# Kernel optimization log

Measured on AMD Instinct MI355X. Metric: run time of the kernel, lower is better.

Reference implementation:

```python
import jax, jax.numpy as jnp
import numpy as np
import math

D_MODEL = 1024
NUM_NEURONS = 2048
LUT_SIZE = 4096
TWO_PI = 2.0 * math.pi


def lut_sin_cos(theta, sin_table, cos_table):
    # Interpolated periodic table lookup over [0, 2*pi)
    n = sin_table.shape[0]
    pos = (theta / TWO_PI) * n
    pos = jnp.mod(pos, n)
    i0 = jnp.floor(pos).astype(jnp.int32)
    frac = pos - i0.astype(theta.dtype)
    i1 = jnp.mod(i0 + 1, n)
    s = sin_table[i0] * (1.0 - frac) + sin_table[i1] * frac
    c = cos_table[i0] * (1.0 - frac) + cos_table[i1] * frac
    return s, c


def setup_inputs() -> dict:
    key = jax.random.key(0)
    ks = jax.random.split(key, 10)
    B = 64
    x_real = jax.random.normal(ks[0], (B, D_MODEL), jnp.float32)
    x_imag = jax.random.normal(ks[1], (B, D_MODEL), jnp.float32)
    t = jax.random.uniform(ks[2], (B,), jnp.float32)
    # xavier_uniform with gain=0.5 for linear weights
    def xavier(k, shape, gain):
        fan_out, fan_in = shape
        a = gain * math.sqrt(6.0 / (fan_in + fan_out))
        return jax.random.uniform(k, shape, jnp.float32, -a, a)
    ic_w = xavier(ks[3], (D_MODEL, 2 * D_MODEL), 0.5)
    ic_b = jnp.zeros((D_MODEL,), jnp.float32)
    W = jax.random.normal(ks[4], (NUM_NEURONS, D_MODEL), jnp.float32) * 0.02
    Bp = jnp.zeros((NUM_NEURONS, D_MODEL), jnp.float32)
    attn_cos = jnp.ones((NUM_NEURONS, D_MODEL), jnp.float32)
    attn_sin = jnp.ones((NUM_NEURONS, D_MODEL), jnp.float32)
    wr = xavier(ks[5], (D_MODEL, NUM_NEURONS), 0.5)
    wi = xavier(ks[6], (D_MODEL, NUM_NEURONS), 0.5)
    grid = jnp.arange(LUT_SIZE, dtype=jnp.float32) * (TWO_PI / LUT_SIZE)
    sin_table = jnp.sin(grid)
    cos_table = jnp.cos(grid)
    return {"x_real": x_real, "x_imag": x_imag, "t": t,
            "ic_w": ic_w, "ic_b": ic_b, "W": W, "Bp": Bp,
            "attn_cos": attn_cos, "attn_sin": attn_sin,
            "wr": wr, "wi": wi,
            "sin_table": sin_table, "cos_table": cos_table}


def reference(x_real, x_imag, t, ic_w, ic_b, W, Bp, attn_cos, attn_sin, wr, wi, sin_table, cos_table):
    x_combined = jnp.concatenate([x_real, x_imag], axis=-1)          # [B, 2D]
    x_collapsed = x_combined @ ic_w.T + ic_b                          # [B, D]
    wavelength = 1.0 + jnp.abs(W)                                     # [N, D]
    theta = x_collapsed[:, None, :] / wavelength + Bp + t[:, None, None]  # [B, N, D]
    sin_t, cos_t = lut_sin_cos(theta, sin_table, cos_table)
    cos_sum = jnp.einsum('bnd,nd->bn', cos_t, attn_cos)               # fused weight+reduce
    sin_sum = jnp.einsum('bnd,nd->bn', sin_t, attn_sin)
    out_real = jax.nn.silu(cos_sum @ wr.T)                            # [B, D]
    out_imag = jax.nn.silu(sin_sum @ wi.T)
    return out_real, out_imag
```

## Files before the change

kernel.cpp:

```cpp
#include <hip/hip_runtime.h>
#include <stdint.h>

#define DM 1024
#define NN 2048
#define BB 64

static constexpr float INV2PI = 0.15915494309189535f;

__device__ __forceinline__ uint32_t bf16r(float x) {
  uint32_t b = __float_as_uint(x);
  b += 0x7fffu + ((b >> 16) & 1u);
  return b >> 16;
}

__global__ __launch_bounds__(256) void k0_prep(
    const float* __restrict__ xr, const float* __restrict__ xi,
    float* __restrict__ xcombP)
{
  __shared__ float tile[64][65];
  int bid = blockIdx.x;
  int t = threadIdx.x;
  int k0 = bid * 64;
  const float* src = (k0 < 1024) ? xr : xi;
  int koff = k0 & 1023;
  int c = t & 63, rl = t >> 6;
#pragma unroll
  for (int i = 0; i < 16; ++i) {
    int b = rl * 16 + i;
    tile[b][c] = src[b * 1024 + koff + c];
  }
  __syncthreads();
  float2* out2 = (float2*)xcombP;
  int bl = t & 63, kp = t >> 6;
#pragma unroll
  for (int i = 0; i < 8; ++i) {
    int kl = (kp * 8 + i) * 2;
    float2 v = make_float2(tile[bl][kl], tile[bl][kl + 1]);
    out2[(size_t)((k0 + kl) >> 1) * 64 + bl] = v;
  }
}

__global__ __launch_bounds__(1024) void k1_collapse(
    const float* __restrict__ xcombP, const float* __restrict__ icw,
    const float* __restrict__ icb, const float* __restrict__ W,
    uint32_t* __restrict__ xcp, float* __restrict__ rinv)
{
  __shared__ float part[16][4][64];
  int bid = blockIdx.x;
  int t = threadIdx.x;
  if (bid >= 256) {
    int j = bid - 256;
    const float4* W4 = (const float4*)W;
    float4* R4 = (float4*)rinv;
    int base = j * 2048 + t;
#pragma unroll
    for (int i = 0; i < 2; ++i) {
      int idx = base + i * 1024;
      float4 w = W4[idx];
      float4 r;
      r.x = 1.0f / (1.0f + fabsf(w.x));
      r.y = 1.0f / (1.0f + fabsf(w.y));
      r.z = 1.0f / (1.0f + fabsf(w.z));
      r.w = 1.0f / (1.0f + fabsf(w.w));
      R4[idx] = r;
    }
    return;
  }
  int d0 = bid * 4;
  int wave = __builtin_amdgcn_readfirstlane((int)(t >> 6));
  int lane = t & 63;
  const float2* P2 = (const float2*)xcombP;
  float acc[4] = {0.f, 0.f, 0.f, 0.f};
  int kbase = wave * 128;
  for (int kk = 0; kk < 128; kk += 4) {
    int k = kbase + kk;
    float2 xa = P2[(size_t)(k >> 1) * 64 + lane];
    float2 xb = P2[(size_t)((k >> 1) + 1) * 64 + lane];
#pragma unroll
    for (int r = 0; r < 4; ++r) {
      float4 w = *(const float4*)(icw + (size_t)(d0 + r) * 2048 + k);
      acc[r] = fmaf(w.x, xa.x, acc[r]);
      acc[r] = fmaf(w.y, xa.y, acc[r]);
      acc[r] = fmaf(w.z, xb.x, acc[r]);
      acc[r] = fmaf(w.w, xb.y, acc[r]);
    }
  }
#pragma unroll
  for (int r = 0; r < 4; ++r) part[wave][r][lane] = acc[r];
  __syncthreads();
  if (t < 128) {
    int pj = t >> 6;
    int b = t & 63;
    float s0 = 0.f, s1 = 0.f;
#pragma unroll
    for (int w = 0; w < 16; ++w) {
      s0 += part[w][2 * pj][b];
      s1 += part[w][2 * pj + 1][b];
    }
    float x0 = (s0 + icb[d0 + 2 * pj]) * INV2PI;
    float x1 = (s1 + icb[d0 + 2 * pj + 1]) * INV2PI;
    uint32_t u = bf16r(x0) | (bf16r(x1) << 16);
    xcp[(size_t)((d0 >> 1) + pj) * 64 + b] = u;
  }
}

#define K2_STEP(r4, b4, a4, s4, xu0, xu1)                                 \
  do {                                                                     \
    float x0 = __uint_as_float((xu0) << 16);                               \
    float x1 = __uint_as_float((xu0) & 0xffff0000u);                       \
    float x2 = __uint_as_float((xu1) << 16);                               \
    float x3 = __uint_as_float((xu1) & 0xffff0000u);                       \
    float rv0 = fmaf(x0, (r4).x, fmaf((b4).x, INV2PI, t2));                \
    accc0 = fmaf(__builtin_amdgcn_cosf(rv0), (a4).x, accc0);               \
    accs0 = fmaf(__builtin_amdgcn_sinf(rv0), (s4).x, accs0);               \
    float rv1 = fmaf(x1, (r4).y, fmaf((b4).y, INV2PI, t2));                \
    accc1 = fmaf(__builtin_amdgcn_cosf(rv1), (a4).y, accc1);               \
    accs1 = fmaf(__builtin_amdgcn_sinf(rv1), (s4).y, accs1);               \
    float rv2 = fmaf(x2, (r4).z, fmaf((b4).z, INV2PI, t2));                \
    accc0 = fmaf(__builtin_amdgcn_cosf(rv2), (a4).z, accc0);               \
    accs0 = fmaf(__builtin_amdgcn_sinf(rv2), (s4).z, accs0);               \
    float rv3 = fmaf(x3, (r4).w, fmaf((b4).w, INV2PI, t2));                \
    accc1 = fmaf(__builtin_amdgcn_cosf(rv3), (a4).w, accc1);               \
    accs1 = fmaf(__builtin_amdgcn_sinf(rv3), (s4).w, accs1);               \
  } while (0)

__global__ __launch_bounds__(512) void k2_resonant(
    const uint32_t* __restrict__ xcp, const float* __restrict__ rinv,
    const float* __restrict__ Bp, const float* __restrict__ ac,
    const float* __restrict__ as_, const float* __restrict__ tin,
    uint32_t* __restrict__ cssP)
{
  __shared__ __align__(16) uint32_t xlds[64][64];
  __shared__ __align__(16) float plds[2][2][8][4][64];
  int wave = __builtin_amdgcn_readfirstlane((int)(threadIdx.x >> 6));
  int lane = threadIdx.x & 63;
  int bid = blockIdx.x;
  int q = bid & 7;
  int n0 = (bid >> 3) * 16 + wave;
  float t2 = tin[lane] * INV2PI;

  const char* xsrc = (const char*)(xcp + (size_t)q * 64 * 64);
  char* xdst = (char*)&xlds[0][0];
#pragma unroll
  for (int r = 0; r < 2; ++r) {
    int j = wave * 2 + r;
    __builtin_amdgcn_global_load_lds(
        (const __attribute__((address_space(1))) void*)(xsrc + j * 1024 + lane * 16),
        (__attribute__((address_space(3))) void*)(xdst + j * 1024), 16, 0, 0);
  }

  int g = lane >> 4;
  const float* ab = (g == 0) ? rinv : (g == 1) ? Bp : (g == 2) ? ac : as_;
#pragma unroll
  for (int h = 0; h < 2; ++h) {
    const float* gp =
        ab + (size_t)(n0 + h * 8) * 1024 + (size_t)q * 128 + (lane & 15) * 4;
#pragma unroll
    for (int c = 0; c < 2; ++c) {
      __builtin_amdgcn_global_load_lds(
          (const __attribute__((address_space(1))) void*)(gp + c * 64),
          (__attribute__((address_space(3))) void*)&plds[h][c][wave][0][0],
          16, 0, 0);
    }
  }

  __syncthreads();

#pragma unroll
  for (int h = 0; h < 2; ++h) {
    float accc0 = 0.f, accs0 = 0.f, accc1 = 0.f, accs1 = 0.f;
#pragma unroll
    for (int c = 0; c < 2; ++c) {
      const float4* pr = (const float4*)&plds[h][c][wave][0][0];
#pragma unroll 4
      for (int i = 0; i < 16; ++i) {
        int ga = c * 16 + i;
        uint32_t xu0 = xlds[2 * ga][lane];
        uint32_t xu1 = xlds[2 * ga + 1][lane];
        float4 r4 = pr[i];
        float4 b4 = pr[16 + i];
        float4 a4 = pr[32 + i];
        float4 s4 = pr[48 + i];
        K2_STEP(r4, b4, a4, s4, xu0, xu1);
      }
    }
    size_t o = ((size_t)q * 2048 + n0 + h * 8) * 64 + lane;
    cssP[o] = bf16r(accc0 + accc1) | (bf16r(accs0 + accs1) << 16);
  }
}

__global__ __launch_bounds__(256) void k2b_reduce(
    const uint32_t* __restrict__ cssP,
    uint32_t* __restrict__ csB, uint32_t* __restrict__ ssB)
{
  int i = blockIdx.x * 256 + threadIdx.x;
  int np = i >> 6, b = i & 63;
  int n0 = 2 * np;
  float c0 = 0.f, c1 = 0.f, s0 = 0.f, s1 = 0.f;
#pragma unroll
  for (int j = 0; j < 8; ++j) {
    size_t base = ((size_t)j * 2048 + n0) * 64 + b;
    uint32_t u0 = cssP[base];
    uint32_t u1 = cssP[base + 64];
    c0 += __uint_as_float(u0 << 16);
    s0 += __uint_as_float(u0 & 0xffff0000u);
    c1 += __uint_as_float(u1 << 16);
    s1 += __uint_as_float(u1 & 0xffff0000u);
  }
  csB[i] = bf16r(c0) | (bf16r(c1) << 16);
  ssB[i] = bf16r(s0) | (bf16r(s1) << 16);
}

__global__ __launch_bounds__(1024) void k3_out(
    const uint32_t* __restrict__ csB, const uint32_t* __restrict__ ssB,
    const float* __restrict__ wr, const float* __restrict__ wi,
    float* __restrict__ out)
{
  __shared__ float part[16][4][65];
  int bid = blockIdx.x;
  int sel = bid >> 8;
  int d0 = (bid & 255) * 4;
  int wave = __builtin_amdgcn_readfirstlane((int)(threadIdx.x >> 6));
  int lane = threadIdx.x & 63;
  const uint32_t* src2 = sel ? ssB : csB;
  const float* wt = sel ? wi : wr;
  float acc[4] = {0.f, 0.f, 0.f, 0.f};
  int n0 = wave * 128;
  for (int i = 0; i < 32; ++i) {
    int n = n0 + i * 4;
    uint32_t xu0 = src2[(size_t)(n >> 1) * 64 + lane];
    uint32_t xu1 = src2[(size_t)((n >> 1) + 1) * 64 + lane];
    float cv0 = __uint_as_float(xu0 << 16);
    float cv1 = __uint_as_float(xu0 & 0xffff0000u);
    float cv2 = __uint_as_float(xu1 << 16);
    float cv3 = __uint_as_float(xu1 & 0xffff0000u);
#pragma unroll
    for (int r = 0; r < 4; ++r) {
      float4 wv = *(const float4*)(wt + (size_t)(d0 + r) * 2048 + n);
      acc[r] = fmaf(cv0, wv.x, acc[r]);
      acc[r] = fmaf(cv1, wv.y, acc[r]);
      acc[r] = fmaf(cv2, wv.z, acc[r]);
      acc[r] = fmaf(cv3, wv.w, acc[r]);
    }
  }
#pragma unroll
  for (int r = 0; r < 4; ++r) part[wave][r][lane] = acc[r];
  __syncthreads();
  int t = threadIdx.x;
  if (t < 256) {
    int b = t >> 2, j = t & 3;
    float s = 0.f;
#pragma unroll
    for (int w = 0; w < 16; ++w) s += part[w][j][b];
    float y = s / (1.0f + __expf(-s));
    out[(size_t)sel * 65536 + (size_t)b * 1024 + d0 + j] = y;
  }
}

extern "C" void kernel_launch(void* const* d_in, const int* in_sizes, int n_in,
                              void* d_out, int out_size, void* d_ws, size_t ws_size,
                              hipStream_t stream) {
  const float* xr  = (const float*)d_in[0];
  const float* xi  = (const float*)d_in[1];
  const float* t   = (const float*)d_in[2];
  const float* icw = (const float*)d_in[3];
  const float* icb = (const float*)d_in[4];
  const float* W   = (const float*)d_in[5];
  const float* Bp  = (const float*)d_in[6];
  const float* ac  = (const float*)d_in[7];
  const float* as_ = (const float*)d_in[8];
  const float* wr  = (const float*)d_in[9];
  const float* wi  = (const float*)d_in[10];

  float* ws = (float*)d_ws;
  float* rinv    = ws;
  float* xcombP  = ws + 2097152;
  uint32_t* xcp  = (uint32_t*)(ws + 2228224);
  uint32_t* cssP = (uint32_t*)(ws + 2260992);
  uint32_t* csB  = (uint32_t*)(ws + 3309568);
  uint32_t* ssB  = (uint32_t*)(ws + 3375104);
  float* out = (float*)d_out;

  k0_prep<<<dim3(32), dim3(256), 0, stream>>>(xr, xi, xcombP);
  k1_collapse<<<dim3(512), dim3(1024), 0, stream>>>(xcombP, icw, icb, W, xcp, rinv);
  k2_resonant<<<dim3(1024), dim3(512), 0, stream>>>(xcp, rinv, Bp, ac, as_, t, cssP);
  k2b_reduce<<<dim3(256), dim3(256), 0, stream>>>(cssP, csB, ssB);
  k3_out<<<dim3(512), dim3(1024), 0, stream>>>(csB, ssB, wr, wi, out);
}
```

Measured before the change: 76.52 us.

## Drop transpose prep kernel and halve per-block work in resonant kernel

Removes the k0_prep transpose kernel. k1_collapse now reads x_real/x_imag directly with float4 loads per batch row, which saves one launch and a workspace round trip but gives strided, uncoalesced x accesses across lanes. Separately, k2_resonant now processes one neuron per wave instead of two, doubling the grid to 2048 blocks. This halves LDS use per block and raises parallelism, at the cost of reloading the x tile twice as often.

```diff
diff --git a/kernel.cpp b/kernel.cpp
--- a/kernel.cpp
+++ b/kernel.cpp
@@ -13,36 +13,10 @@
   return b >> 16;
 }
 
-__global__ __launch_bounds__(256) void k0_prep(
+__global__ __launch_bounds__(1024) void k1_collapse(
     const float* __restrict__ xr, const float* __restrict__ xi,
-    float* __restrict__ xcombP)
-{
-  __shared__ float tile[64][65];
-  int bid = blockIdx.x;
-  int t = threadIdx.x;
-  int k0 = bid * 64;
-  const float* src = (k0 < 1024) ? xr : xi;
-  int koff = k0 & 1023;
-  int c = t & 63, rl = t >> 6;
-#pragma unroll
-  for (int i = 0; i < 16; ++i) {
-    int b = rl * 16 + i;
-    tile[b][c] = src[b * 1024 + koff + c];
-  }
-  __syncthreads();
-  float2* out2 = (float2*)xcombP;
-  int bl = t & 63, kp = t >> 6;
-#pragma unroll
-  for (int i = 0; i < 8; ++i) {
-    int kl = (kp * 8 + i) * 2;
-    float2 v = make_float2(tile[bl][kl], tile[bl][kl + 1]);
-    out2[(size_t)((k0 + kl) >> 1) * 64 + bl] = v;
-  }
-}
-
-__global__ __launch_bounds__(1024) void k1_collapse(
-    const float* __restrict__ xcombP, const float* __restrict__ icw,
-    const float* __restrict__ icb, const float* __restrict__ W,
+    const float* __restrict__ icw, const float* __restrict__ icb,
+    const float* __restrict__ W,
     uint32_t* __restrict__ xcp, float* __restrict__ rinv)
 {
   __shared__ float part[16][4][64];
@@ -69,20 +43,20 @@
   int d0 = bid * 4;
   int wave = __builtin_amdgcn_readfirstlane((int)(t >> 6));
   int lane = t & 63;
-  const float2* P2 = (const float2*)xcombP;
+  const float* src = (wave < 8) ? xr : xi;
+  int kbase = (wave & 7) * 128;
+  int kgofs = (wave < 8) ? 0 : 1024;
   float acc[4] = {0.f, 0.f, 0.f, 0.f};
-  int kbase = wave * 128;
   for (int kk = 0; kk < 128; kk += 4) {
     int k = kbase + kk;
-    float2 xa = P2[(size_t)(k >> 1) * 64 + lane];
-    float2 xb = P2[(size_t)((k >> 1) + 1) * 64 + lane];
+    float4 xv = *(const float4*)(src + (size_t)lane * 1024 + k);
 #pragma unroll
     for (int r = 0; r < 4; ++r) {
-      float4 w = *(const float4*)(icw + (size_t)(d0 + r) * 2048 + k);
-      acc[r] = fmaf(w.x, xa.x, acc[r]);
-      acc[r] = fmaf(w.y, xa.y, acc[r]);
-      acc[r] = fmaf(w.z, xb.x, acc[r]);
-      acc[r] = fmaf(w.w, xb.y, acc[r]);
+      float4 w = *(const float4*)(icw + (size_t)(d0 + r) * 2048 + kgofs + k);
+      acc[r] = fmaf(w.x, xv.x, acc[r]);
+      acc[r] = fmaf(w.y, xv.y, acc[r]);
+      acc[r] = fmaf(w.z, xv.z, acc[r]);
+      acc[r] = fmaf(w.w, xv.w, acc[r]);
     }
   }
 #pragma unroll
@@ -131,12 +105,12 @@
     uint32_t* __restrict__ cssP)
 {
   __shared__ __align__(16) uint32_t xlds[64][64];
-  __shared__ __align__(16) float plds[2][2][8][4][64];
+  __shared__ __align__(16) float plds[2][8][4][64];
   int wave = __builtin_amdgcn_readfirstlane((int)(threadIdx.x >> 6));
   int lane = threadIdx.x & 63;
   int bid = blockIdx.x;
   int q = bid & 7;
-  int n0 = (bid >> 3) * 16 + wave;
+  int n = (bid >> 3) * 8 + wave;
   float t2 = tin[lane] * INV2PI;
 
   const char* xsrc = (const char*)(xcp + (size_t)q * 64 * 64);
@@ -151,42 +125,36 @@
 
   int g = lane >> 4;
   const float* ab = (g == 0) ? rinv : (g == 1) ? Bp : (g == 2) ? ac : as_;
-#pragma unroll
-  for (int h = 0; h < 2; ++h) {
-    const float* gp =
-        ab + (size_t)(n0 + h * 8) * 1024 + (size_t)q * 128 + (lane & 15) * 4;
-#pragma unroll
-    for (int c = 0; c < 2; ++c) {
-      __builtin_amdgcn_global_load_lds(
-          (const __attribute__((address_space(1))) void*)(gp + c * 64),
-          (__attribute__((address_space(3))) void*)&plds[h][c][wave][0][0],
-          16, 0, 0);
-    }
+  const float* gp = ab + (size_t)n * 1024 + (size_t)q * 128 + (lane & 15) * 4;
+#pragma unroll
+  for (int c = 0; c < 2; ++c) {
+    __builtin_amdgcn_global_load_lds(
+        (const __attribute__((address_space(1))) void*)(gp + c * 64),
+        (__attribute__((address_space(3))) void*)&plds[c][wave][0][0], 16, 0, 0);
   }
 
   __syncthreads();
 
-#pragma unroll
-  for (int h = 0; h < 2; ++h) {
-    float accc0 = 0.f, accs0 = 0.f, accc1 = 0.f, accs1 = 0.f;
-#pragma unroll
-    for (int c = 0; c < 2; ++c) {
-      const float4* pr = (const float4*)&plds[h][c][wave][0][0];
+  float accc0 = 0.f, accs0 = 0.f, accc1 = 0.f, accs1 = 0.f;
+
+#pragma unroll
+  for (int c = 0; c < 2; ++c) {
+    const float4* pr = (const float4*)&plds[c][wave][0][0];
 #pragma unroll 4
-      for (int i = 0; i < 16; ++i) {
-        int ga = c * 16 + i;
-        uint32_t xu0 = xlds[2 * ga][lane];
-        uint32_t xu1 = xlds[2 * ga + 1][lane];
-        float4 r4 = pr[i];
-        float4 b4 = pr[16 + i];
-        float4 a4 = pr[32 + i];
-        float4 s4 = pr[48 + i];
-        K2_STEP(r4, b4, a4, s4, xu0, xu1);
-      }
-    }
-    size_t o = ((size_t)q * 2048 + n0 + h * 8) * 64 + lane;
-    cssP[o] = bf16r(accc0 + accc1) | (bf16r(accs0 + accs1) << 16);
-  }
+    for (int i = 0; i < 16; ++i) {
+      int ga = c * 16 + i;
+      uint32_t xu0 = xlds[2 * ga][lane];
+      uint32_t xu1 = xlds[2 * ga + 1][lane];
+      float4 r4 = pr[i];
+      float4 b4 = pr[16 + i];
+      float4 a4 = pr[32 + i];
+      float4 s4 = pr[48 + i];
+      K2_STEP(r4, b4, a4, s4, xu0, xu1);
+    }
+  }
+
+  size_t o = ((size_t)q * 2048 + n) * 64 + lane;
+  cssP[o] = bf16r(accc0 + accc1) | (bf16r(accs0 + accs1) << 16);
 }
 
 __global__ __launch_bounds__(256) void k2b_reduce(
@@ -274,16 +242,14 @@
 
   float* ws = (float*)d_ws;
   float* rinv    = ws;
-  float* xcombP  = ws + 2097152;
-  uint32_t* xcp  = (uint32_t*)(ws + 2228224);
-  uint32_t* cssP = (uint32_t*)(ws + 2260992);
-  uint32_t* csB  = (uint32_t*)(ws + 3309568);
-  uint32_t* ssB  = (uint32_t*)(ws + 3375104);
+  uint32_t* xcp  = (uint32_t*)(ws + 2097152);
+  uint32_t* cssP = (uint32_t*)(ws + 2129920);
+  uint32_t* csB  = (uint32_t*)(ws + 3178496);
+  uint32_t* ssB  = (uint32_t*)(ws + 3244032);
   float* out = (float*)d_out;
 
-  k0_prep<<<dim3(32), dim3(256), 0, stream>>>(xr, xi, xcombP);
-  k1_collapse<<<dim3(512), dim3(1024), 0, stream>>>(xcombP, icw, icb, W, xcp, rinv);
-  k2_resonant<<<dim3(1024), dim3(512), 0, stream>>>(xcp, rinv, Bp, ac, as_, t, cssP);
+  k1_collapse<<<dim3(512), dim3(1024), 0, stream>>>(xr, xi, icw, icb, W, xcp, rinv);
+  k2_resonant<<<dim3(2048), dim3(512), 0, stream>>>(xcp, rinv, Bp, ac, as_, t, cssP);
   k2b_reduce<<<dim3(256), dim3(256), 0, stream>>>(cssP, csB, ssB);
   k3_out<<<dim3(512), dim3(1024), 0, stream>>>(csB, ssB, wr, wi, out);
 }
```

Measured after the change: 79.23 us. +3.5%, slower.

## Halve per-block neuron work in resonant kernel and prefetch activations in GEMV loops

Applied to the files above, without the earlier changes.

The resonant kernel now handles one neuron row per wave instead of two and launches twice as many blocks. This halves the parameter LDS footprint per block and spreads the work across more workgroups, but each block has to load the shared x tile again, which doubles that traffic. The collapse and output GEMV loops also register-prefetch the next activation pair one iteration ahead. On the last iteration this prefetch issues a redundant wrap-around load.

```diff
diff --git a/kernel.cpp b/kernel.cpp
--- a/kernel.cpp
+++ b/kernel.cpp
@@ -72,10 +72,13 @@
   const float2* P2 = (const float2*)xcombP;
   float acc[4] = {0.f, 0.f, 0.f, 0.f};
   int kbase = wave * 128;
+  float2 xa = P2[(size_t)(kbase >> 1) * 64 + lane];
+  float2 xb = P2[(size_t)((kbase >> 1) + 1) * 64 + lane];
   for (int kk = 0; kk < 128; kk += 4) {
     int k = kbase + kk;
-    float2 xa = P2[(size_t)(k >> 1) * 64 + lane];
-    float2 xb = P2[(size_t)((k >> 1) + 1) * 64 + lane];
+    int kn = (kk < 124) ? (k + 4) : kbase;
+    float2 na = P2[(size_t)(kn >> 1) * 64 + lane];
+    float2 nb = P2[(size_t)((kn >> 1) + 1) * 64 + lane];
 #pragma unroll
     for (int r = 0; r < 4; ++r) {
       float4 w = *(const float4*)(icw + (size_t)(d0 + r) * 2048 + k);
@@ -84,6 +87,7 @@
       acc[r] = fmaf(w.z, xb.x, acc[r]);
       acc[r] = fmaf(w.w, xb.y, acc[r]);
     }
+    xa = na; xb = nb;
   }
 #pragma unroll
   for (int r = 0; r < 4; ++r) part[wave][r][lane] = acc[r];
@@ -131,12 +135,12 @@
     uint32_t* __restrict__ cssP)
 {
   __shared__ __align__(16) uint32_t xlds[64][64];
-  __shared__ __align__(16) float plds[2][2][8][4][64];
+  __shared__ __align__(16) float plds[2][8][4][64];
   int wave = __builtin_amdgcn_readfirstlane((int)(threadIdx.x >> 6));
   int lane = threadIdx.x & 63;
   int bid = blockIdx.x;
   int q = bid & 7;
-  int n0 = (bid >> 3) * 16 + wave;
+  int n = (bid >> 3) * 8 + wave;
   float t2 = tin[lane] * INV2PI;
 
   const char* xsrc = (const char*)(xcp + (size_t)q * 64 * 64);
@@ -151,42 +155,36 @@
 
   int g = lane >> 4;
   const float* ab = (g == 0) ? rinv : (g == 1) ? Bp : (g == 2) ? ac : as_;
-#pragma unroll
-  for (int h = 0; h < 2; ++h) {
-    const float* gp =
-        ab + (size_t)(n0 + h * 8) * 1024 + (size_t)q * 128 + (lane & 15) * 4;
-#pragma unroll
-    for (int c = 0; c < 2; ++c) {
-      __builtin_amdgcn_global_load_lds(
-          (const __attribute__((address_space(1))) void*)(gp + c * 64),
-          (__attribute__((address_space(3))) void*)&plds[h][c][wave][0][0],
-          16, 0, 0);
-    }
-  }
-
-  __syncthreads();
-
-#pragma unroll
-  for (int h = 0; h < 2; ++h) {
-    float accc0 = 0.f, accs0 = 0.f, accc1 = 0.f, accs1 = 0.f;
-#pragma unroll
-    for (int c = 0; c < 2; ++c) {
-      const float4* pr = (const float4*)&plds[h][c][wave][0][0];
+  const float* gp = ab + (size_t)n * 1024 + (size_t)q * 128 + (lane & 15) * 4;
+#pragma unroll
+  for (int c = 0; c < 2; ++c) {
+    __builtin_amdgcn_global_load_lds(
+        (const __attribute__((address_space(1))) void*)(gp + c * 64),
+        (__attribute__((address_space(3))) void*)&plds[c][wave][0][0], 16, 0, 0);
+  }
+
+  __syncthreads();
+
+  float accc0 = 0.f, accs0 = 0.f, accc1 = 0.f, accs1 = 0.f;
+
+#pragma unroll
+  for (int c = 0; c < 2; ++c) {
+    const float4* pr = (const float4*)&plds[c][wave][0][0];
 #pragma unroll 4
-      for (int i = 0; i < 16; ++i) {
-        int ga = c * 16 + i;
-        uint32_t xu0 = xlds[2 * ga][lane];
-        uint32_t xu1 = xlds[2 * ga + 1][lane];
-        float4 r4 = pr[i];
-        float4 b4 = pr[16 + i];
-        float4 a4 = pr[32 + i];
-        float4 s4 = pr[48 + i];
-        K2_STEP(r4, b4, a4, s4, xu0, xu1);
-      }
-    }
-    size_t o = ((size_t)q * 2048 + n0 + h * 8) * 64 + lane;
-    cssP[o] = bf16r(accc0 + accc1) | (bf16r(accs0 + accs1) << 16);
-  }
+    for (int i = 0; i < 16; ++i) {
+      int ga = c * 16 + i;
+      uint32_t xu0 = xlds[2 * ga][lane];
+      uint32_t xu1 = xlds[2 * ga + 1][lane];
+      float4 r4 = pr[i];
+      float4 b4 = pr[16 + i];
+      float4 a4 = pr[32 + i];
+      float4 s4 = pr[48 + i];
+      K2_STEP(r4, b4, a4, s4, xu0, xu1);
+    }
+  }
+
+  size_t o = ((size_t)q * 2048 + n) * 64 + lane;
+  cssP[o] = bf16r(accc0 + accc1) | (bf16r(accs0 + accs1) << 16);
 }
 
 __global__ __launch_bounds__(256) void k2b_reduce(
@@ -226,10 +224,13 @@
   const float* wt = sel ? wi : wr;
   float acc[4] = {0.f, 0.f, 0.f, 0.f};
   int n0 = wave * 128;
+  uint32_t xu0 = src2[(size_t)(n0 >> 1) * 64 + lane];
+  uint32_t xu1 = src2[(size_t)((n0 >> 1) + 1) * 64 + lane];
   for (int i = 0; i < 32; ++i) {
     int n = n0 + i * 4;
-    uint32_t xu0 = src2[(size_t)(n >> 1) * 64 + lane];
-    uint32_t xu1 = src2[(size_t)((n >> 1) + 1) * 64 + lane];
+    int nn = (i < 31) ? (n + 4) : n0;
+    uint32_t nu0 = src2[(size_t)(nn >> 1) * 64 + lane];
+    uint32_t nu1 = src2[(size_t)((nn >> 1) + 1) * 64 + lane];
     float cv0 = __uint_as_float(xu0 << 16);
     float cv1 = __uint_as_float(xu0 & 0xffff0000u);
     float cv2 = __uint_as_float(xu1 << 16);
@@ -242,6 +243,7 @@
       acc[r] = fmaf(cv2, wv.z, acc[r]);
       acc[r] = fmaf(cv3, wv.w, acc[r]);
     }
+    xu0 = nu0; xu1 = nu1;
   }
 #pragma unroll
   for (int r = 0; r < 4; ++r) part[wave][r][lane] = acc[r];
@@ -283,7 +285,7 @@
 
   k0_prep<<<dim3(32), dim3(256), 0, stream>>>(xr, xi, xcombP);
   k1_collapse<<<dim3(512), dim3(1024), 0, stream>>>(xcombP, icw, icb, W, xcp, rinv);
-  k2_resonant<<<dim3(1024), dim3(512), 0, stream>>>(xcp, rinv, Bp, ac, as_, t, cssP);
+  k2_resonant<<<dim3(2048), dim3(512), 0, stream>>>(xcp, rinv, Bp, ac, as_, t, cssP);
   k2b_reduce<<<dim3(256), dim3(256), 0, stream>>>(cssP, csB, ssB);
   k3_out<<<dim3(512), dim3(1024), 0, stream>>>(csB, ssB, wr, wi, out);
 }
```

Measured after the change: 83.52 us. +9.1%, slower.

## Pack per-neuron parameters into bf16 pairs and shrink resonant kernel blocks

Applied to the files above, without the earlier changes.

The prep stage now reads W, Bp, attn_cos and attn_sin and writes two packed bf16x2 arrays (1/wavelength with Bp/2π, and cos-weight with sin-weight), replacing the single fp32 rinv array. The resonant kernel loads one 16-byte chunk per lane from these packed arrays, so it reads half the parameter bytes. Each block now handles 8 neurons instead of 16, and the grid is twice as large. The packing kernel has more blocks and reads all four parameter tensors, so that extra pass costs something in exchange. Rounding Bp and the attention weights to bf16 adds some precision loss.

```diff
diff --git a/kernel.cpp b/kernel.cpp
--- a/kernel.cpp
+++ b/kernel.cpp
@@ -43,27 +43,31 @@
 __global__ __launch_bounds__(1024) void k1_collapse(
     const float* __restrict__ xcombP, const float* __restrict__ icw,
     const float* __restrict__ icb, const float* __restrict__ W,
-    uint32_t* __restrict__ xcp, float* __restrict__ rinv)
+    const float* __restrict__ Bp, const float* __restrict__ ac,
+    const float* __restrict__ as_,
+    uint32_t* __restrict__ xcp, uint32_t* __restrict__ pk1,
+    uint32_t* __restrict__ pk2)
 {
   __shared__ float part[16][4][64];
   int bid = blockIdx.x;
   int t = threadIdx.x;
   if (bid >= 256) {
-    int j = bid - 256;
-    const float4* W4 = (const float4*)W;
-    float4* R4 = (float4*)rinv;
-    int base = j * 2048 + t;
-#pragma unroll
-    for (int i = 0; i < 2; ++i) {
-      int idx = base + i * 1024;
-      float4 w = W4[idx];
-      float4 r;
-      r.x = 1.0f / (1.0f + fabsf(w.x));
-      r.y = 1.0f / (1.0f + fabsf(w.y));
-      r.z = 1.0f / (1.0f + fabsf(w.z));
-      r.w = 1.0f / (1.0f + fabsf(w.w));
-      R4[idx] = r;
-    }
+    int idx = (bid - 256) * 1024 + t;
+    float4 w = ((const float4*)W)[idx];
+    float4 bp = ((const float4*)Bp)[idx];
+    float4 a = ((const float4*)ac)[idx];
+    float4 s = ((const float4*)as_)[idx];
+    uint4 o1, o2;
+    o1.x = bf16r(1.0f / (1.0f + fabsf(w.x))) | (bf16r(bp.x * INV2PI) << 16);
+    o1.y = bf16r(1.0f / (1.0f + fabsf(w.y))) | (bf16r(bp.y * INV2PI) << 16);
+    o1.z = bf16r(1.0f / (1.0f + fabsf(w.z))) | (bf16r(bp.z * INV2PI) << 16);
+    o1.w = bf16r(1.0f / (1.0f + fabsf(w.w))) | (bf16r(bp.w * INV2PI) << 16);
+    o2.x = bf16r(a.x) | (bf16r(s.x) << 16);
+    o2.y = bf16r(a.y) | (bf16r(s.y) << 16);
+    o2.z = bf16r(a.z) | (bf16r(s.z) << 16);
+    o2.w = bf16r(a.w) | (bf16r(s.w) << 16);
+    ((uint4*)pk1)[idx] = o1;
+    ((uint4*)pk2)[idx] = o2;
     return;
   }
   int d0 = bid * 4;
@@ -104,39 +108,18 @@
   }
 }
 
-#define K2_STEP(r4, b4, a4, s4, xu0, xu1)                                 \
-  do {                                                                     \
-    float x0 = __uint_as_float((xu0) << 16);                               \
-    float x1 = __uint_as_float((xu0) & 0xffff0000u);                       \
-    float x2 = __uint_as_float((xu1) << 16);                               \
-    float x3 = __uint_as_float((xu1) & 0xffff0000u);                       \
-    float rv0 = fmaf(x0, (r4).x, fmaf((b4).x, INV2PI, t2));                \
-    accc0 = fmaf(__builtin_amdgcn_cosf(rv0), (a4).x, accc0);               \
-    accs0 = fmaf(__builtin_amdgcn_sinf(rv0), (s4).x, accs0);               \
-    float rv1 = fmaf(x1, (r4).y, fmaf((b4).y, INV2PI, t2));                \
-    accc1 = fmaf(__builtin_amdgcn_cosf(rv1), (a4).y, accc1);               \
-    accs1 = fmaf(__builtin_amdgcn_sinf(rv1), (s4).y, accs1);               \
-    float rv2 = fmaf(x2, (r4).z, fmaf((b4).z, INV2PI, t2));                \
-    accc0 = fmaf(__builtin_amdgcn_cosf(rv2), (a4).z, accc0);               \
-    accs0 = fmaf(__builtin_amdgcn_sinf(rv2), (s4).z, accs0);               \
-    float rv3 = fmaf(x3, (r4).w, fmaf((b4).w, INV2PI, t2));                \
-    accc1 = fmaf(__builtin_amdgcn_cosf(rv3), (a4).w, accc1);               \
-    accs1 = fmaf(__builtin_amdgcn_sinf(rv3), (s4).w, accs1);               \
-  } while (0)
-
 __global__ __launch_bounds__(512) void k2_resonant(
-    const uint32_t* __restrict__ xcp, const float* __restrict__ rinv,
-    const float* __restrict__ Bp, const float* __restrict__ ac,
-    const float* __restrict__ as_, const float* __restrict__ tin,
+    const uint32_t* __restrict__ xcp, const uint32_t* __restrict__ pk1,
+    const uint32_t* __restrict__ pk2, const float* __restrict__ tin,
     uint32_t* __restrict__ cssP)
 {
   __shared__ __align__(16) uint32_t xlds[64][64];
-  __shared__ __align__(16) float plds[2][2][8][4][64];
+  __shared__ __align__(16) uint32_t plds[8][256];
   int wave = __builtin_amdgcn_readfirstlane((int)(threadIdx.x >> 6));
   int lane = threadIdx.x & 63;
   int bid = blockIdx.x;
   int q = bid & 7;
-  int n0 = (bid >> 3) * 16 + wave;
+  int n = (bid >> 3) * 8 + wave;
   float t2 = tin[lane] * INV2PI;
 
   const char* xsrc = (const char*)(xcp + (size_t)q * 64 * 64);
@@ -149,44 +132,52 @@
         (__attribute__((address_space(3))) void*)(xdst + j * 1024), 16, 0, 0);
   }
 
-  int g = lane >> 4;
-  const float* ab = (g == 0) ? rinv : (g == 1) ? Bp : (g == 2) ? ac : as_;
-#pragma unroll
-  for (int h = 0; h < 2; ++h) {
-    const float* gp =
-        ab + (size_t)(n0 + h * 8) * 1024 + (size_t)q * 128 + (lane & 15) * 4;
-#pragma unroll
-    for (int c = 0; c < 2; ++c) {
-      __builtin_amdgcn_global_load_lds(
-          (const __attribute__((address_space(1))) void*)(gp + c * 64),
-          (__attribute__((address_space(3))) void*)&plds[h][c][wave][0][0],
-          16, 0, 0);
-    }
-  }
-
-  __syncthreads();
-
-#pragma unroll
-  for (int h = 0; h < 2; ++h) {
-    float accc0 = 0.f, accs0 = 0.f, accc1 = 0.f, accs1 = 0.f;
-#pragma unroll
-    for (int c = 0; c < 2; ++c) {
-      const float4* pr = (const float4*)&plds[h][c][wave][0][0];
+  const uint32_t* psrc = (lane < 32) ? pk1 : pk2;
+  const uint32_t* gp = psrc + (size_t)n * 1024 + (size_t)q * 128 + (lane & 31) * 4;
+  __builtin_amdgcn_global_load_lds(
+      (const __attribute__((address_space(1))) void*)gp,
+      (__attribute__((address_space(3))) void*)&plds[wave][0], 16, 0, 0);
+
+  __syncthreads();
+
+  float accc0 = 0.f, accs0 = 0.f, accc1 = 0.f, accs1 = 0.f;
+  const uint4* pr1 = (const uint4*)&plds[wave][0];
+  const uint4* pr2 = (const uint4*)&plds[wave][128];
+
 #pragma unroll 4
-      for (int i = 0; i < 16; ++i) {
-        int ga = c * 16 + i;
-        uint32_t xu0 = xlds[2 * ga][lane];
-        uint32_t xu1 = xlds[2 * ga + 1][lane];
-        float4 r4 = pr[i];
-        float4 b4 = pr[16 + i];
-        float4 a4 = pr[32 + i];
-        float4 s4 = pr[48 + i];
-        K2_STEP(r4, b4, a4, s4, xu0, xu1);
-      }
-    }
-    size_t o = ((size_t)q * 2048 + n0 + h * 8) * 64 + lane;
-    cssP[o] = bf16r(accc0 + accc1) | (bf16r(accs0 + accs1) << 16);
-  }
+  for (int i = 0; i < 32; ++i) {
+    uint32_t xu0 = xlds[2 * i][lane];
+    uint32_t xu1 = xlds[2 * i + 1][lane];
+    uint4 p1 = pr1[i];
+    uint4 p2 = pr2[i];
+    float x0 = __uint_as_float(xu0 << 16);
+    float x1 = __uint_as_float(xu0 & 0xffff0000u);
+    float x2 = __uint_as_float(xu1 << 16);
+    float x3 = __uint_as_float(xu1 & 0xffff0000u);
+
+    float rv0 = fmaf(x0, __uint_as_float(p1.x << 16),
+                     t2 + __uint_as_float(p1.x & 0xffff0000u));
+    accc0 = fmaf(__builtin_amdgcn_cosf(rv0), __uint_as_float(p2.x << 16), accc0);
+    accs0 = fmaf(__builtin_amdgcn_sinf(rv0), __uint_as_float(p2.x & 0xffff0000u), accs0);
+
+    float rv1 = fmaf(x1, __uint_as_float(p1.y << 16),
+                     t2 + __uint_as_float(p1.y & 0xffff0000u));
+    accc1 = fmaf(__builtin_amdgcn_cosf(rv1), __uint_as_float(p2.y << 16), accc1);
+    accs1 = fmaf(__builtin_amdgcn_sinf(rv1), __uint_as_float(p2.y & 0xffff0000u), accs1);
+
+    float rv2 = fmaf(x2, __uint_as_float(p1.z << 16),
+                     t2 + __uint_as_float(p1.z & 0xffff0000u));
+    accc0 = fmaf(__builtin_amdgcn_cosf(rv2), __uint_as_float(p2.z << 16), accc0);
+    accs0 = fmaf(__builtin_amdgcn_sinf(rv2), __uint_as_float(p2.z & 0xffff0000u), accs0);
+
+    float rv3 = fmaf(x3, __uint_as_float(p1.w << 16),
+                     t2 + __uint_as_float(p1.w & 0xffff0000u));
+    accc1 = fmaf(__builtin_amdgcn_cosf(rv3), __uint_as_float(p2.w << 16), accc1);
+    accs1 = fmaf(__builtin_amdgcn_sinf(rv3), __uint_as_float(p2.w & 0xffff0000u), accs1);
+  }
+
+  size_t o = ((size_t)q * 2048 + n) * 64 + lane;
+  cssP[o] = bf16r(accc0 + accc1) | (bf16r(accs0 + accs1) << 16);
 }
 
 __global__ __launch_bounds__(256) void k2b_reduce(
@@ -273,17 +264,18 @@
   const float* wi  = (const float*)d_in[10];
 
   float* ws = (float*)d_ws;
-  float* rinv    = ws;
-  float* xcombP  = ws + 2097152;
-  uint32_t* xcp  = (uint32_t*)(ws + 2228224);
-  uint32_t* cssP = (uint32_t*)(ws + 2260992);
-  uint32_t* csB  = (uint32_t*)(ws + 3309568);
-  uint32_t* ssB  = (uint32_t*)(ws + 3375104);
+  uint32_t* pk1  = (uint32_t*)ws;
+  uint32_t* pk2  = (uint32_t*)(ws + 2097152);
+  float* xcombP  = ws + 4194304;
+  uint32_t* xcp  = (uint32_t*)(ws + 4325376);
+  uint32_t* cssP = (uint32_t*)(ws + 4358144);
+  uint32_t* csB  = (uint32_t*)(ws + 5406720);
+  uint32_t* ssB  = (uint32_t*)(ws + 5472256);
   float* out = (float*)d_out;
 
   k0_prep<<<dim3(32), dim3(256), 0, stream>>>(xr, xi, xcombP);
-  k1_collapse<<<dim3(512), dim3(1024), 0, stream>>>(xcombP, icw, icb, W, xcp, rinv);
-  k2_resonant<<<dim3(1024), dim3(512), 0, stream>>>(xcp, rinv, Bp, ac, as_, t, cssP);
+  k1_collapse<<<dim3(768), dim3(1024), 0, stream>>>(xcombP, icw, icb, W, Bp, ac, as_, xcp, pk1, pk2);
+  k2_resonant<<<dim3(2048), dim3(512), 0, stream>>>(xcp, pk1, pk2, t, cssP);
   k2b_reduce<<<dim3(256), dim3(256), 0, stream>>>(cssP, csB, ssB);
   k3_out<<<dim3(512), dim3(1024), 0, stream>>>(csB, ssB, wr, wi, out);
 }
```

Result: slower. 85.32 us (+11.5%).
